# Optimization experiments

Hardware: AMD Instinct MI355X
Metric: run time of the kernel (lower is better)

The kernel has to match this reference:

```python
import jax, jax.numpy as jnp
import numpy as np

NH, DK, W = 16, 64, 128        # n_heads, head_dim, sliding window
D = NH * DK                    # d_model = 1024
NEG = -1.0e9


def setup_inputs() -> dict:
    key = jax.random.key(0)
    k0, k1, k2, k3, k4 = jax.random.split(key, 5)
    L, B, T0 = 128, 8, 4096
    x_chunk = jax.random.normal(k0, (L, B, D), jnp.float32)
    K_cache = jax.random.normal(k1, (T0, B, NH, DK), jnp.float32)
    V_cache = jax.random.normal(k2, (T0, B, NH, DK), jnp.float32)
    s = 1.0 / np.sqrt(D)
    qkv_w = jax.random.normal(k3, (D, 3 * D), jnp.float32) * s
    qkv_b = jnp.zeros((3 * D,), jnp.float32)
    out_w = jax.random.normal(k4, (D, D), jnp.float32) * s
    out_b = jnp.zeros((D,), jnp.float32)
    return {"x_chunk": x_chunk, "K_cache": K_cache, "V_cache": V_cache,
            "qkv_w": qkv_w, "qkv_b": qkv_b, "out_w": out_w, "out_b": out_b}


def reference(x_chunk, K_cache, V_cache, qkv_w, qkv_b, out_w, out_b):
    L, B, Dm = x_chunk.shape
    qkv = (x_chunk @ qkv_w + qkv_b).reshape(L, B, 3, NH, DK)
    q, k, v = qkv[:, :, 0], qkv[:, :, 1], qkv[:, :, 2]
    K = jnp.concatenate([K_cache, k], axis=0)   # [T,B,nh,dk]
    V = jnp.concatenate([V_cache, v], axis=0)
    T = K.shape[0]
    idx = jnp.arange(T)
    # causal mask over global positions (rows = absolute key positions)
    mask = jnp.where(idx[None, :] > idx[:, None], NEG, 0.0)   # [T,T]
    if T > W:  # static shape -> Python if is fine under jit
        valid = jnp.zeros((T,), jnp.float32).at[-W:].set(1.0)
        mask = mask + (1.0 - valid[None, :]) * NEG
    # scores: [B,nh,L,T]
    logits = jnp.einsum('lbhd,tbhd->bhlt', q, K) / np.sqrt(DK)
    logits = logits + mask[-L:, :][None, None]
    weights = jax.nn.softmax(logits, axis=-1)
    o = jnp.einsum('bhlt,tbhd->lbhd', weights, V).reshape(L, B, Dm)
    y = o @ out_w + out_b
    return (y, K, V)
```

## Files before the change

kernel.cpp:

```cpp
#include <hip/hip_runtime.h>

#define L_CHUNK 128
#define BATCH   8
#define NHEADS  16
#define DKDIM   64
#define DMODEL  1024
#define T0CACHE 4096
#define TTOT    4224
#define ROWSTR  8192

typedef __attribute__((ext_vector_type(8))) __bf16 bf16x8;
typedef __attribute__((ext_vector_type(4))) float f32x4;
typedef __attribute__((ext_vector_type(8))) unsigned short us8;

__device__ __forceinline__ unsigned short f2bf(float f) {
    unsigned int u = __float_as_uint(f);
    u += 0x7fffu + ((u >> 16) & 1u);
    return (unsigned short)(u >> 16);
}

__global__ __launch_bounds__(256) void prep_convert(
        const float* __restrict__ x, const float* __restrict__ qkv_w,
        const float* __restrict__ out_w,
        unsigned short* __restrict__ xb, unsigned short* __restrict__ wb,
        unsigned short* __restrict__ owb) {
    int idx = blockIdx.x * 256 + threadIdx.x;
    const float4* s4; ushort4* d4; int rel;
    if (idx < 262144)        { s4 = (const float4*)x;     d4 = (ushort4*)xb;  rel = idx; }
    else if (idx < 1048576)  { s4 = (const float4*)qkv_w; d4 = (ushort4*)wb;  rel = idx - 262144; }
    else                     { s4 = (const float4*)out_w; d4 = (ushort4*)owb; rel = idx - 1048576; }
    float4 v = s4[rel];
    ushort4 o; o.x = f2bf(v.x); o.y = f2bf(v.y); o.z = f2bf(v.z); o.w = f2bf(v.w);
    d4[rel] = o;
}

template<int MODE>
__device__ __forceinline__ void gemm_body(
        int bx, int by,
        const unsigned short* __restrict__ A,
        const unsigned short* __restrict__ B,
        const float* __restrict__ bias,
        float* __restrict__ Cf, unsigned short* __restrict__ Cq,
        float* __restrict__ C1, float* __restrict__ C2,
        int K, int N) {
    __shared__ unsigned short Al[64][40];
    __shared__ unsigned short Bl[64][40];

    const int tid  = threadIdx.x;
    const int wave = tid >> 6;
    const int lane = tid & 63;
    const int m0 = by * 64;
    const int n0 = bx * 64;

    f32x4 zero = {0.f, 0.f, 0.f, 0.f};
    f32x4 acc[4];
    #pragma unroll
    for (int i = 0; i < 4; ++i) acc[i] = zero;

    const int ar = tid >> 2, ac = (tid & 3) * 8;
    const int bk = tid >> 3, bn = (tid & 7) * 8;
    const int rot = tid & 7;
    const int mrow = wave * 16 + (lane & 15);
    const int koff = (lane >> 4) * 8;

    for (int k0 = 0; k0 < K; k0 += 32) {
        us8 av = *(const us8*)(A + (size_t)(m0 + ar) * K + (k0 + ac));
        us8 bv = *(const us8*)(B + (size_t)(k0 + bk) * N + (n0 + bn));
        *(us8*)(&Al[ar][ac]) = av;
        #pragma unroll
        for (int i = 0; i < 8; ++i) {
            int ii = (i + rot) & 7;
            Bl[bn + ii][bk] = bv[ii];
        }
        __syncthreads();
        bf16x8 af = __builtin_bit_cast(bf16x8, *(const us8*)(&Al[mrow][koff]));
        #pragma unroll
        for (int nt = 0; nt < 4; ++nt) {
            bf16x8 bf = __builtin_bit_cast(bf16x8,
                            *(const us8*)(&Bl[nt * 16 + (lane & 15)][koff]));
            acc[nt] = __builtin_amdgcn_mfma_f32_16x16x32_bf16(af, bf, acc[nt], 0, 0, 0);
        }
        __syncthreads();
    }

    const int colt  = lane & 15;
    const int rbase = (lane >> 4) * 4;
    #pragma unroll
    for (int nt = 0; nt < 4; ++nt) {
        int gcol = n0 + nt * 16 + colt;
        float bval = bias[gcol];
        #pragma unroll
        for (int r = 0; r < 4; ++r) {
            int grow = m0 + wave * 16 + rbase + r;
            float val = acc[nt][r] + bval;
            if (MODE == 0) {
                Cf[(size_t)grow * N + gcol] = val;
            } else {
                int s = gcol >> 10, w = gcol & 1023;
                int l = grow >> 3, b = grow & 7;
                size_t kvoff = (size_t)(T0CACHE + l) * ROWSTR + (size_t)b * DMODEL + w;
                if (s == 0)      Cq[(size_t)grow * DMODEL + w] = f2bf(val);
                else if (s == 1) C1[kvoff] = val;
                else             C2[kvoff] = val;
            }
        }
    }
}

__global__ __launch_bounds__(256) void qkv_and_copy(
        const unsigned short* __restrict__ xb,
        const unsigned short* __restrict__ wb,
        const float* __restrict__ qkv_b,
        unsigned short* __restrict__ qb,
        float* __restrict__ Kout, float* __restrict__ Vout,
        const float4* __restrict__ Kc, const float4* __restrict__ Vc) {
    const int g = blockIdx.x;
    const bool isGemm = (g < 3072) && ((g & 3) == 0);
    if (isGemm) {
        int gi = g >> 2;
        gemm_body<1>(gi % 48, gi / 48, xb, wb, qkv_b, nullptr, qb, Kout, Vout,
                     DMODEL, 3 * DMODEL);
    } else {
        int cid = (g < 3072) ? (g - (g >> 2) - 1) : (g - 768);
        const int stride = 2560 * 256;
        float4* Kd = (float4*)Kout;
        float4* Vd = (float4*)Vout;
        for (int e = cid * 256 + threadIdx.x; e < 8388608; e += stride) Kd[e] = Kc[e];
        for (int e = cid * 256 + threadIdx.x; e < 8388608; e += stride) Vd[e] = Vc[e];
    }
}

__global__ __launch_bounds__(256) void out_gemm(
        const unsigned short* __restrict__ ob,
        const unsigned short* __restrict__ owb,
        const float* __restrict__ out_b, float* __restrict__ y) {
    gemm_body<0>(blockIdx.x, blockIdx.y, ob, owb, out_b, y, nullptr, nullptr, nullptr,
                 DMODEL, DMODEL);
}

__global__ __launch_bounds__(256) void attn_mfma(
        const unsigned short* __restrict__ qb,
        const float* __restrict__ Kout,
        const float* __restrict__ Vout,
        unsigned short* __restrict__ ob) {
    __shared__ unsigned short Kb[128][72];
    __shared__ unsigned short Vt[64][136];
    __shared__ unsigned short Pb[4][16][136];

    const int tid  = threadIdx.x;
    const int wave = tid >> 6, lane = tid & 63;
    const int qh = blockIdx.x & 1, bh = blockIdx.x >> 1;
    const int b = bh >> 4, h = bh & 15;
    const int q0 = qh * 64;
    const size_t base = (size_t)T0CACHE * ROWSTR + (size_t)b * DMODEL + h * DKDIM;

    for (int e = tid; e < 2048; e += 256) {
        int j = e >> 4, d4 = (e & 15) * 4;
        float4 kv = *(const float4*)(Kout + base + (size_t)j * ROWSTR + d4);
        ushort4 u; u.x = f2bf(kv.x); u.y = f2bf(kv.y); u.z = f2bf(kv.z); u.w = f2bf(kv.w);
        *(ushort4*)&Kb[j][d4] = u;
        float4 vv = *(const float4*)(Vout + base + (size_t)j * ROWSTR + d4);
        Vt[d4 + 0][j] = f2bf(vv.x); Vt[d4 + 1][j] = f2bf(vv.y);
        Vt[d4 + 2][j] = f2bf(vv.z); Vt[d4 + 3][j] = f2bf(vv.w);
    }

    const int qrow = q0 + wave * 16 + (lane & 15);
    const size_t arow = (size_t)(qrow * 8 + b) * DMODEL + h * DKDIM;
    bf16x8 qa0 = __builtin_bit_cast(bf16x8, *(const us8*)(qb + arow + (lane >> 4) * 8));
    bf16x8 qa1 = __builtin_bit_cast(bf16x8, *(const us8*)(qb + arow + 32 + (lane >> 4) * 8));
    __syncthreads();

    f32x4 sacc[8];
    f32x4 zero = {0.f, 0.f, 0.f, 0.f};
    #pragma unroll
    for (int t = 0; t < 8; ++t) sacc[t] = zero;
    #pragma unroll
    for (int t = 0; t < 8; ++t) {
        bf16x8 k0 = __builtin_bit_cast(bf16x8,
                        *(const us8*)(&Kb[t * 16 + (lane & 15)][(lane >> 4) * 8]));
        bf16x8 k1 = __builtin_bit_cast(bf16x8,
                        *(const us8*)(&Kb[t * 16 + (lane & 15)][32 + (lane >> 4) * 8]));
        sacc[t] = __builtin_amdgcn_mfma_f32_16x16x32_bf16(qa0, k0, sacc[t], 0, 0, 0);
        sacc[t] = __builtin_amdgcn_mfma_f32_16x16x32_bf16(qa1, k1, sacc[t], 0, 0, 0);
    }

    const int col = lane & 15;
    float mrow[4], lsum[4], inv[4];
    #pragma unroll
    for (int r = 0; r < 4; ++r) mrow[r] = -3e38f;
    #pragma unroll
    for (int t = 0; t < 8; ++t) {
        #pragma unroll
        for (int r = 0; r < 4; ++r) {
            int key = t * 16 + col;
            int qi  = q0 + wave * 16 + (lane >> 4) * 4 + r;
            float v = sacc[t][r] * 0.125f;
            if (key > qi) v = -1e9f;
            sacc[t][r] = v;
            mrow[r] = fmaxf(mrow[r], v);
        }
    }
    #pragma unroll
    for (int r = 0; r < 4; ++r) {
        #pragma unroll
        for (int off = 1; off < 16; off <<= 1)
            mrow[r] = fmaxf(mrow[r], __shfl_xor(mrow[r], off, 64));
        lsum[r] = 0.f;
    }
    #pragma unroll
    for (int t = 0; t < 8; ++t) {
        #pragma unroll
        for (int r = 0; r < 4; ++r) {
            float p = __expf(sacc[t][r] - mrow[r]);
            lsum[r] += p;
            Pb[wave][(lane >> 4) * 4 + r][t * 16 + col] = f2bf(p);
        }
    }
    #pragma unroll
    for (int r = 0; r < 4; ++r) {
        #pragma unroll
        for (int off = 1; off < 16; off <<= 1)
            lsum[r] += __shfl_xor(lsum[r], off, 64);
        inv[r] = 1.f / lsum[r];
    }
    __syncthreads();

    bf16x8 pa[4];
    #pragma unroll
    for (int ks = 0; ks < 4; ++ks)
        pa[ks] = __builtin_bit_cast(bf16x8,
                     *(const us8*)(&Pb[wave][lane & 15][ks * 32 + (lane >> 4) * 8]));
    f32x4 oacc[4];
    #pragma unroll
    for (int n = 0; n < 4; ++n) oacc[n] = zero;
    #pragma unroll
    for (int n = 0; n < 4; ++n) {
        #pragma unroll
        for (int ks = 0; ks < 4; ++ks) {
            bf16x8 vb = __builtin_bit_cast(bf16x8,
                            *(const us8*)(&Vt[n * 16 + (lane & 15)][ks * 32 + (lane >> 4) * 8]));
            oacc[n] = __builtin_amdgcn_mfma_f32_16x16x32_bf16(pa[ks], vb, oacc[n], 0, 0, 0);
        }
    }

    #pragma unroll
    for (int n = 0; n < 4; ++n) {
        #pragma unroll
        for (int r = 0; r < 4; ++r) {
            int qi = q0 + wave * 16 + (lane >> 4) * 4 + r;
            int d  = n * 16 + col;
            ob[(size_t)(qi * 8 + b) * DMODEL + h * DKDIM + d] = f2bf(oacc[n][r] * inv[r]);
        }
    }
}

extern "C" void kernel_launch(void* const* d_in, const int* in_sizes, int n_in,
                              void* d_out, int out_size, void* d_ws, size_t ws_size,
                              hipStream_t stream) {
    const float* x     = (const float*)d_in[0];
    const float* Kc    = (const float*)d_in[1];
    const float* Vc    = (const float*)d_in[2];
    const float* qkv_w = (const float*)d_in[3];
    const float* qkv_b = (const float*)d_in[4];
    const float* out_w = (const float*)d_in[5];
    const float* out_b = (const float*)d_in[6];

    float* y    = (float*)d_out;
    float* Kout = y + (size_t)L_CHUNK * BATCH * DMODEL;
    float* Vout = Kout + (size_t)TTOT * ROWSTR;

    char* ws = (char*)d_ws;
    unsigned short* xb  = (unsigned short*)ws;
    unsigned short* wb  = (unsigned short*)(ws + (size_t)(2  << 20));
    unsigned short* owb = (unsigned short*)(ws + (size_t)(8  << 20));
    unsigned short* qb  = (unsigned short*)(ws + (size_t)(10 << 20));
    unsigned short* ob  = (unsigned short*)(ws + (size_t)(12 << 20));

    prep_convert<<<5120, 256, 0, stream>>>(x, qkv_w, out_w, xb, wb, owb);

    qkv_and_copy<<<3328, 256, 0, stream>>>(xb, wb, qkv_b, qb, Kout, Vout,
                                           (const float4*)Kc, (const float4*)Vc);

    attn_mfma<<<256, 256, 0, stream>>>(qb, Kout, Vout, ob);

    out_gemm<<<dim3(16, 16), 256, 0, stream>>>(ob, owb, out_b, y);
}
```

Baseline: 522.4 us.

## Fuse bf16 conversion into GEMM loads and spread cache copy across kernels

Removes the separate prep_convert kernel: the QKV and output GEMMs now read fp32 inputs and weights directly and convert to bf16 while loading tiles. The K/V cache copy is split into three slices, run by extra blocks in the QKV, attention and output-projection kernels, so the bandwidth-bound copy overlaps all stages. This saves one launch and the bf16 staging round trip. In exchange, GEMM blocks re-read fp32 weights (twice the bytes) and convert them redundantly per tile.

```diff
diff --git a/kernel.cpp b/kernel.cpp
--- a/kernel.cpp
+++ b/kernel.cpp
@@ -9,6 +9,10 @@
 #define TTOT    4224
 #define ROWSTR  8192
 
+#define N8PER   8388608u
+#define SPLIT1  5242880u
+#define SPLIT2  6815744u
+
 typedef __attribute__((ext_vector_type(8))) __bf16 bf16x8;
 typedef __attribute__((ext_vector_type(4))) float f32x4;
 typedef __attribute__((ext_vector_type(8))) unsigned short us8;
@@ -19,26 +23,21 @@
     return (unsigned short)(u >> 16);
 }
 
-__global__ __launch_bounds__(256) void prep_convert(
-        const float* __restrict__ x, const float* __restrict__ qkv_w,
-        const float* __restrict__ out_w,
-        unsigned short* __restrict__ xb, unsigned short* __restrict__ wb,
-        unsigned short* __restrict__ owb) {
-    int idx = blockIdx.x * 256 + threadIdx.x;
-    const float4* s4; ushort4* d4; int rel;
-    if (idx < 262144)        { s4 = (const float4*)x;     d4 = (ushort4*)xb;  rel = idx; }
-    else if (idx < 1048576)  { s4 = (const float4*)qkv_w; d4 = (ushort4*)wb;  rel = idx - 262144; }
-    else                     { s4 = (const float4*)out_w; d4 = (ushort4*)owb; rel = idx - 1048576; }
-    float4 v = s4[rel];
-    ushort4 o; o.x = f2bf(v.x); o.y = f2bf(v.y); o.z = f2bf(v.z); o.w = f2bf(v.w);
-    d4[rel] = o;
-}
-
-template<int MODE>
+__device__ __forceinline__ void copy_slice(int cid, int ncopy,
+        unsigned e0, unsigned e1,
+        float4* __restrict__ Kd, const float4* __restrict__ Kc,
+        float4* __restrict__ Vd, const float4* __restrict__ Vc) {
+    const unsigned stride = (unsigned)ncopy * 256u;
+    const unsigned base = e0 + (unsigned)cid * 256u + threadIdx.x;
+    for (unsigned e = base; e < e1; e += stride) Kd[e] = Kc[e];
+    for (unsigned e = base; e < e1; e += stride) Vd[e] = Vc[e];
+}
+
+template<int MODE, bool AF32, bool BF32>
 __device__ __forceinline__ void gemm_body(
         int bx, int by,
-        const unsigned short* __restrict__ A,
-        const unsigned short* __restrict__ B,
+        const void* __restrict__ Ap,
+        const void* __restrict__ Bp,
         const float* __restrict__ bias,
         float* __restrict__ Cf, unsigned short* __restrict__ Cq,
         float* __restrict__ C1, float* __restrict__ C2,
@@ -64,8 +63,27 @@
     const int koff = (lane >> 4) * 8;
 
     for (int k0 = 0; k0 < K; k0 += 32) {
-        us8 av = *(const us8*)(A + (size_t)(m0 + ar) * K + (k0 + ac));
-        us8 bv = *(const us8*)(B + (size_t)(k0 + bk) * N + (n0 + bn));
+        us8 av, bv;
+        if constexpr (AF32) {
+            const float* A = (const float*)Ap;
+            const float4 a0 = *(const float4*)(A + (size_t)(m0 + ar) * K + (k0 + ac));
+            const float4 a1 = *(const float4*)(A + (size_t)(m0 + ar) * K + (k0 + ac) + 4);
+            av[0] = f2bf(a0.x); av[1] = f2bf(a0.y); av[2] = f2bf(a0.z); av[3] = f2bf(a0.w);
+            av[4] = f2bf(a1.x); av[5] = f2bf(a1.y); av[6] = f2bf(a1.z); av[7] = f2bf(a1.w);
+        } else {
+            const unsigned short* A = (const unsigned short*)Ap;
+            av = *(const us8*)(A + (size_t)(m0 + ar) * K + (k0 + ac));
+        }
+        if constexpr (BF32) {
+            const float* B = (const float*)Bp;
+            const float4 b0 = *(const float4*)(B + (size_t)(k0 + bk) * N + (n0 + bn));
+            const float4 b1 = *(const float4*)(B + (size_t)(k0 + bk) * N + (n0 + bn) + 4);
+            bv[0] = f2bf(b0.x); bv[1] = f2bf(b0.y); bv[2] = f2bf(b0.z); bv[3] = f2bf(b0.w);
+            bv[4] = f2bf(b1.x); bv[5] = f2bf(b1.y); bv[6] = f2bf(b1.z); bv[7] = f2bf(b1.w);
+        } else {
+            const unsigned short* B = (const unsigned short*)Bp;
+            bv = *(const us8*)(B + (size_t)(k0 + bk) * N + (n0 + bn));
+        }
         *(us8*)(&Al[ar][ac]) = av;
         #pragma unroll
         for (int i = 0; i < 8; ++i) {
@@ -108,8 +126,8 @@
 }
 
 __global__ __launch_bounds__(256) void qkv_and_copy(
-        const unsigned short* __restrict__ xb,
-        const unsigned short* __restrict__ wb,
+        const float* __restrict__ x,
+        const float* __restrict__ qkv_w,
         const float* __restrict__ qkv_b,
         unsigned short* __restrict__ qb,
         float* __restrict__ Kout, float* __restrict__ Vout,
@@ -118,34 +136,29 @@
     const bool isGemm = (g < 3072) && ((g & 3) == 0);
     if (isGemm) {
         int gi = g >> 2;
-        gemm_body<1>(gi % 48, gi / 48, xb, wb, qkv_b, nullptr, qb, Kout, Vout,
-                     DMODEL, 3 * DMODEL);
+        gemm_body<1, true, true>(gi % 48, gi / 48, x, qkv_w, qkv_b,
+                                 nullptr, qb, Kout, Vout, DMODEL, 3 * DMODEL);
     } else {
         int cid = (g < 3072) ? (g - (g >> 2) - 1) : (g - 768);
-        const int stride = 2560 * 256;
-        float4* Kd = (float4*)Kout;
-        float4* Vd = (float4*)Vout;
-        for (int e = cid * 256 + threadIdx.x; e < 8388608; e += stride) Kd[e] = Kc[e];
-        for (int e = cid * 256 + threadIdx.x; e < 8388608; e += stride) Vd[e] = Vc[e];
-    }
-}
-
-__global__ __launch_bounds__(256) void out_gemm(
-        const unsigned short* __restrict__ ob,
-        const unsigned short* __restrict__ owb,
-        const float* __restrict__ out_b, float* __restrict__ y) {
-    gemm_body<0>(blockIdx.x, blockIdx.y, ob, owb, out_b, y, nullptr, nullptr, nullptr,
-                 DMODEL, DMODEL);
+        copy_slice(cid, 2560, 0u, SPLIT1, (float4*)Kout, Kc, (float4*)Vout, Vc);
+    }
 }
 
 __global__ __launch_bounds__(256) void attn_mfma(
         const unsigned short* __restrict__ qb,
         const float* __restrict__ Kout,
         const float* __restrict__ Vout,
-        unsigned short* __restrict__ ob) {
+        unsigned short* __restrict__ ob,
+        const float4* __restrict__ Kc, const float4* __restrict__ Vc) {
     __shared__ unsigned short Kb[128][72];
     __shared__ unsigned short Vt[64][136];
     __shared__ unsigned short Pb[4][16][136];
+
+    if (blockIdx.x >= 256) {
+        copy_slice(blockIdx.x - 256, 768, SPLIT1, SPLIT2,
+                   (float4*)Kout, Kc, (float4*)Vout, Vc);
+        return;
+    }
 
     const int tid  = threadIdx.x;
     const int wave = tid >> 6, lane = tid & 63;
@@ -252,6 +265,22 @@
             ob[(size_t)(qi * 8 + b) * DMODEL + h * DKDIM + d] = f2bf(oacc[n][r] * inv[r]);
         }
     }
+}
+
+__global__ __launch_bounds__(256) void out_gemm(
+        const unsigned short* __restrict__ ob,
+        const float* __restrict__ out_w,
+        const float* __restrict__ out_b, float* __restrict__ y,
+        float* __restrict__ Kout, float* __restrict__ Vout,
+        const float4* __restrict__ Kc, const float4* __restrict__ Vc) {
+    const int g = blockIdx.x;
+    if (g >= 256) {
+        copy_slice(g - 256, 768, SPLIT2, N8PER,
+                   (float4*)Kout, Kc, (float4*)Vout, Vc);
+        return;
+    }
+    gemm_body<0, false, true>(g & 15, g >> 4, ob, out_w, out_b,
+                              y, nullptr, nullptr, nullptr, DMODEL, DMODEL);
 }
 
 extern "C" void kernel_launch(void* const* d_in, const int* in_sizes, int n_in,
@@ -270,18 +299,15 @@
     float* Vout = Kout + (size_t)TTOT * ROWSTR;
 
     char* ws = (char*)d_ws;
-    unsigned short* xb  = (unsigned short*)ws;
-    unsigned short* wb  = (unsigned short*)(ws + (size_t)(2  << 20));
-    unsigned short* owb = (unsigned short*)(ws + (size_t)(8  << 20));
-    unsigned short* qb  = (unsigned short*)(ws + (size_t)(10 << 20));
-    unsigned short* ob  = (unsigned short*)(ws + (size_t)(12 << 20));
-
-    prep_convert<<<5120, 256, 0, stream>>>(x, qkv_w, out_w, xb, wb, owb);
-
-    qkv_and_copy<<<3328, 256, 0, stream>>>(xb, wb, qkv_b, qb, Kout, Vout,
+    unsigned short* qb = (unsigned short*)ws;
+    unsigned short* ob = (unsigned short*)(ws + (size_t)(2 << 20));
+
+    qkv_and_copy<<<3328, 256, 0, stream>>>(x, qkv_w, qkv_b, qb, Kout, Vout,
                                            (const float4*)Kc, (const float4*)Vc);
 
-    attn_mfma<<<256, 256, 0, stream>>>(qb, Kout, Vout, ob);
-
-    out_gemm<<<dim3(16, 16), 256, 0, stream>>>(ob, owb, out_b, y);
-}
+    attn_mfma<<<1024, 256, 0, stream>>>(qb, Kout, Vout, ob,
+                                        (const float4*)Kc, (const float4*)Vc);
+
+    out_gemm<<<1024, 256, 0, stream>>>(ob, out_w, out_b, y, Kout, Vout,
+                                       (const float4*)Kc, (const float4*)Vc);
+}
```

Result: slower. 572.3 us (+9.6%).
